# Optimization experiments

Hardware: AMD Instinct MI355X
Metric: run time of the kernel (lower is better)

Reference implementation:

```python
import jax, jax.numpy as jnp
import numpy as np

T, B, V = 2048, 256, 90   # max_length, batch, pitch classes
P = V - 1                 # 89 pattern channels
IGNORE = 999
EPS = 1e-28


def setup_inputs() -> dict:
    key = jax.random.key(0)
    k1, k2, k3, k4, k5 = jax.random.split(key, 5)
    return {
        "first_scores": jax.random.normal(k1, (T, B, V), dtype=jnp.float32),
        "pattern_scores": jax.random.uniform(k2, (T, B, P), dtype=jnp.float32),
        "first_targs": jax.random.randint(k3, (T, B), 0, V),
        "pattern_targs": jax.random.uniform(k4, (T, B, P), dtype=jnp.float32),
        "lengths": jax.random.randint(k5, (B,), 0, T),
    }


def reference(first_scores, pattern_scores, first_targs, pattern_targs, lengths):
    # CrossEntropyLoss(reduction='none', ignore_index=999) on [T*B, 90] -> [T, B]
    logp = jax.nn.log_softmax(first_scores, axis=-1)
    valid = (first_targs != IGNORE)
    targs_c = jnp.clip(first_targs, 0, V - 1)
    first_losses = -jnp.take_along_axis(logp, targs_c[..., None], axis=-1)[..., 0]
    first_losses = first_losses * valid.astype(first_losses.dtype)

    # Vectorized mask: mask[j, i, k] = 1 iff j < lengths[i] and k < 89 - first_targs[j, i]
    k = jnp.arange(P)                                             # [P]
    len_mask = jnp.arange(T)[:, None] < lengths[None, :]          # [T, B]
    mask = (k[None, None, :] < (P - first_targs)[:, :, None]) & len_mask[:, :, None]
    mask = mask.astype(pattern_scores.dtype)

    # Masked BCE over pattern channels
    pattern_losses = -(pattern_targs * jnp.log(pattern_scores + EPS)
                       + (1.0 - pattern_targs) * jnp.log(1.0 - pattern_scores + EPS))
    pattern_losses = (pattern_losses * mask).sum(axis=2)          # [T, B]

    losses = first_losses + pattern_losses
    return losses.sum() / B
```

## Files before the change

kernel.cpp:

```cpp
#include <hip/hip_runtime.h>

constexpr int T = 2048;
constexpr int B = 256;
constexpr int V = 90;
constexpr int P = 89;
constexpr int IGNORE = 999;
constexpr float EPS = 1e-28f;

__global__ __launch_bounds__(256) void trans_inv_loss_kernel(
    const float* __restrict__ first_scores,
    const float* __restrict__ pattern_scores,
    const int*   __restrict__ first_targs,
    const float* __restrict__ pattern_targs,
    const int*   __restrict__ lengths,
    float*       __restrict__ out)
{
    const int lane   = threadIdx.x & 63;
    const int gwave  = (blockIdx.x * blockDim.x + threadIdx.x) >> 6;
    const int nwaves = (gridDim.x * blockDim.x) >> 6;

    float acc = 0.0f;

    for (int row = gwave; row < T * B; row += nwaves) {
        const int t = row >> 8;
        const int b = row & (B - 1);

        const int targ = first_targs[row];

        const float* fs = first_scores + (size_t)row * V;
        float e = 0.0f;
        if (lane < V / 2) {
            const float2 x = *(const float2*)(fs + lane * 2);
            e = __expf(x.x) + __expf(x.y);
        }
        #pragma unroll
        for (int off = 32; off > 0; off >>= 1)
            e += __shfl_xor(e, off, 64);

        if (targ != IGNORE) {
            float st = fs[targ];
            if (lane == 0) acc += __logf(e) - st;
        }

        if (t < lengths[b]) {
            const int kmax = P - targ;
            const float* ps = pattern_scores + (size_t)row * P;
            const float* pt = pattern_targs  + (size_t)row * P;
            for (int k = lane; k < kmax; k += 64) {
                float p = ps[k];
                float y = pt[k];
                float l1 = __logf(p + EPS);
                float l2 = __logf(1.0f - p + EPS);
                acc -= y * (l1 - l2) + l2;
            }
        }
    }

    #pragma unroll
    for (int off = 32; off > 0; off >>= 1)
        acc += __shfl_xor(acc, off, 64);

    if (lane == 0)
        atomicAdd(out, acc * (1.0f / (float)B));
}

extern "C" void kernel_launch(void* const* d_in, const int* in_sizes, int n_in,
                              void* d_out, int out_size, void* d_ws, size_t ws_size,
                              hipStream_t stream) {
    const float* first_scores   = (const float*)d_in[0];
    const float* pattern_scores = (const float*)d_in[1];
    const int*   first_targs    = (const int*)  d_in[2];
    const float* pattern_targs  = (const float*)d_in[3];
    const int*   lengths        = (const int*)  d_in[4];
    float* out = (float*)d_out;

    hipMemsetAsync(out, 0, sizeof(float) * (size_t)out_size, stream);

    dim3 block(256);
    dim3 grid(2048);
    trans_inv_loss_kernel<<<grid, block, 0, stream>>>(
        first_scores, pattern_scores, first_targs, pattern_targs, lengths, out);
}
```

Measured before the change: 574.6 us.

## Map one thread per row instead of one wavefront per row

Moves from one wavefront per (t,b) row to one thread per row. Each thread loops serially over the 90 logits and the masked pattern channels, and a block-level shared-memory reduction now feeds one atomic per block. The aim is to drop the cross-lane shuffle reductions and the idle lanes of the wave-per-row layout. In exchange, global loads become strided across lanes (uncoalesced), and the variable pattern-loop length causes divergence within a wave.

```diff
diff --git a/kernel.cpp b/kernel.cpp
--- a/kernel.cpp
+++ b/kernel.cpp
@@ -15,53 +15,57 @@
     const int*   __restrict__ lengths,
     float*       __restrict__ out)
 {
-    const int lane   = threadIdx.x & 63;
-    const int gwave  = (blockIdx.x * blockDim.x + threadIdx.x) >> 6;
-    const int nwaves = (gridDim.x * blockDim.x) >> 6;
+    const int row = blockIdx.x * blockDim.x + threadIdx.x;
 
-    float acc = 0.0f;
+    float loss = 0.0f;
 
-    for (int row = gwave; row < T * B; row += nwaves) {
+    if (row < T * B) {
         const int t = row >> 8;
         const int b = row & (B - 1);
 
         const int targ = first_targs[row];
+        const int len  = lengths[b];
 
         const float* fs = first_scores + (size_t)row * V;
-        float e = 0.0f;
-        if (lane < V / 2) {
-            const float2 x = *(const float2*)(fs + lane * 2);
-            e = __expf(x.x) + __expf(x.y);
+        float st = fs[targ];
+        float s = 0.0f;
+        #pragma unroll 9
+        for (int j = 0; j < V / 2; ++j) {
+            const float2 x = *(const float2*)(fs + 2 * j);
+            s += __expf(x.x) + __expf(x.y);
         }
-        #pragma unroll
-        for (int off = 32; off > 0; off >>= 1)
-            e += __shfl_xor(e, off, 64);
+        if (targ != IGNORE)
+            loss = __logf(s) - st;
 
-        if (targ != IGNORE) {
-            float st = fs[targ];
-            if (lane == 0) acc += __logf(e) - st;
-        }
-
-        if (t < lengths[b]) {
+        if (t < len) {
             const int kmax = P - targ;
             const float* ps = pattern_scores + (size_t)row * P;
             const float* pt = pattern_targs  + (size_t)row * P;
-            for (int k = lane; k < kmax; k += 64) {
+            #pragma unroll 4
+            for (int k = 0; k < kmax; ++k) {
                 float p = ps[k];
                 float y = pt[k];
                 float l1 = __logf(p + EPS);
                 float l2 = __logf(1.0f - p + EPS);
-                acc -= y * (l1 - l2) + l2;
+                loss -= y * (l1 - l2) + l2;
             }
         }
     }
 
     #pragma unroll
     for (int off = 32; off > 0; off >>= 1)
-        acc += __shfl_xor(acc, off, 64);
+        loss += __shfl_xor(loss, off, 64);
 
-    if (lane == 0)
-        atomicAdd(out, acc * (1.0f / (float)B));
+    __shared__ float warp_sums[4];
+    const int lane = threadIdx.x & 63;
+    const int wid  = threadIdx.x >> 6;
+    if (lane == 0) warp_sums[wid] = loss;
+    __syncthreads();
+
+    if (threadIdx.x == 0) {
+        float s = warp_sums[0] + warp_sums[1] + warp_sums[2] + warp_sums[3];
+        atomicAdd(out, s * (1.0f / (float)B));
+    }
 }
 
 extern "C" void kernel_launch(void* const* d_in, const int* in_sizes, int n_in,
@@ -77,7 +81,7 @@
     hipMemsetAsync(out, 0, sizeof(float) * (size_t)out_size, stream);
 
     dim3 block(256);
-    dim3 grid(2048);
+    dim3 grid((T * B + 255) / 256);
     trans_inv_loss_kernel<<<grid, block, 0, stream>>>(
         first_scores, pattern_scores, first_targs, pattern_targs, lengths, out);
 }
```

Result: faster. 504.0 us (-12.3%).
